# Kernel tuning notes

Hardware: AMD Instinct MI355X
Metric: run time of the kernel (lower is better)

Reference implementation:

```python
import jax, jax.numpy as jnp
import numpy as np

B, N, HID = 2, 512, 768
BIAF = 256
CLS = 14
CH = 32
SIZE_DIM = 25
N_POS = 30
HSZ = 2 * (BIAF + 1) + SIZE_DIM


def setup_inputs() -> dict:
    key = jax.random.key(0)
    ks = jax.random.split(key, 16)
    s = 0.02
    return {
        "x": jax.random.normal(ks[0], (B, N, HID), jnp.float32),
        "y": jax.random.normal(ks[1], (B, N, HID), jnp.float32),
        "z": jax.random.normal(ks[2], (B, N, N, CH), jnp.float32),
        "mlp1_w": jax.random.normal(ks[3], (BIAF, HID), jnp.float32) * s,
        "mlp1_b": jnp.zeros((BIAF,), jnp.float32),
        "mlp2_w": jax.random.normal(ks[4], (BIAF, HID), jnp.float32) * s,
        "mlp2_b": jnp.zeros((BIAF,), jnp.float32),
        "head_w": jax.random.normal(ks[5], (BIAF, HID), jnp.float32) * s,
        "head_b": jnp.zeros((BIAF,), jnp.float32),
        "tail_w": jax.random.normal(ks[6], (BIAF, HID), jnp.float32) * s,
        "tail_b": jnp.zeros((BIAF,), jnp.float32),
        "biaf_W": jax.random.normal(ks[7], (CLS, BIAF + 1, BIAF + 1), jnp.float32) * s,
        "W": jax.random.normal(ks[8], (CLS, HSZ), jnp.float32) * s,
        "size_emb": jax.random.normal(ks[9], (N_POS, SIZE_DIM), jnp.float32) * s,
    }


def reference(x, y, z, mlp1_w, mlp1_b, mlp2_w, mlp2_b, head_w, head_b,
              tail_w, tail_b, biaf_W, W, size_emb):
    # MLP branches (dropout=0 at eval; torch GELU is exact erf)
    h = jax.nn.gelu(x @ mlp1_w.T + mlp1_b, approximate=False)   # (b,m,BIAF)
    t = jax.nn.gelu(y @ mlp2_w.T + mlp2_b, approximate=False)   # (b,n,BIAF)
    ones = jnp.ones(h.shape[:-1] + (1,), h.dtype)
    h1 = jnp.concatenate([h, ones], -1)                          # (b,m,BIAF+1)
    t1 = jnp.concatenate([t, ones], -1)                          # (b,n,BIAF+1)
    # Biaffine with bias_x=bias_y=True -> (b,cls,m,n)
    o1 = jnp.einsum('bmi,kij,bnj->bkmn', h1, biaf_W, t1)

    # head/tail MLPs with LeakyReLU(0.01), then append 1-column
    head = jax.nn.leaky_relu(x @ head_w.T + head_b, 0.01)
    tail = jax.nn.leaky_relu(x @ tail_w.T + tail_b, 0.01)
    head = jnp.concatenate([head, ones], -1)                     # (b,m,BIAF+1)
    tail = jnp.concatenate([tail, ones], -1)                     # (b,n,BIAF+1)

    # einsum('bmnh,kh->bkmn', cat([head_m, tail_n, size_mn]), W) decomposed so
    # the (b,m,n,HSZ) pairwise tensor is never materialized (same math).
    d = head.shape[-1]
    Wh, Wt, Ws = W[:, :d], W[:, d:2 * d], W[:, 2 * d:]
    n = x.shape[1]
    ar = jnp.arange(n)
    ids = jnp.clip(ar[None, :] - ar[:, None], -N_POS // 2, N_POS // 2 - 1) + N_POS // 2
    se = size_emb[ids]                                           # (m,n,SIZE_DIM)
    o3 = (jnp.einsum('bmh,kh->bkm', head, Wh)[:, :, :, None]
          + jnp.einsum('bnh,kh->bkn', tail, Wt)[:, :, None, :]
          + jnp.einsum('mnh,kh->kmn', se, Ws)[None])
    return o1 + o3
```

## Files before the change

kernel.cpp:

```cpp
#include <hip/hip_runtime.h>
#include <hip/hip_bf16.h>
#include <math.h>
#include <stdint.h>

#define BDIM 2
#define NDIM 512
#define HID 768
#define BIAF 256
#define CLS 14
#define DD 257
#define NPOS 30
#define SDIM 25
#define HSZ 539
#define PK 288
#define PJ 384

typedef unsigned short ushort_t;
typedef __attribute__((ext_vector_type(8))) short short8;
typedef __attribute__((ext_vector_type(4))) float floatx4;
typedef __attribute__((ext_vector_type(4))) unsigned short ushort4_t;

#define MFMA16(a, b, c) __builtin_amdgcn_mfma_f32_16x16x32_bf16((a), (b), (c), 0, 0, 0)

__device__ inline float bf2f(ushort_t u) {
    union { unsigned int i; float f; } c; c.i = ((unsigned)u) << 16; return c.f;
}
__device__ inline ushort_t f2bf(float f) {
    __hip_bfloat16 h = __float2bfloat16(f);
    return *(ushort_t*)&h;
}

__device__ inline int xcd_swz(int bid, int nwg) {
    int q = nwg >> 3;
    return (bid & 7) * q + (bid >> 3);
}

__device__ inline void glds16(const ushort_t* g, const ushort_t* l) {
    __builtin_amdgcn_global_load_lds(
        (const __attribute__((address_space(1))) unsigned int*)(unsigned long long)(uintptr_t)g,
        (__attribute__((address_space(3))) unsigned int*)(unsigned int)(uintptr_t)l,
        16, 0, 0);
}


__global__ __launch_bounds__(256) void prep_all(
    const float* __restrict__ biafW, ushort_t* __restrict__ packW,
    const float* __restrict__ x, const float* __restrict__ y,
    const float* __restrict__ m1w, const float* __restrict__ m2w,
    const float* __restrict__ hw,  const float* __restrict__ tw,
    ushort_t* __restrict__ xhi, ushort_t* __restrict__ xlo,
    ushort_t* __restrict__ yhi, ushort_t* __restrict__ ylo,
    ushort_t* __restrict__ whi, ushort_t* __restrict__ wlo,
    ushort_t* __restrict__ h1hi, ushort_t* __restrict__ h1lo,
    ushort_t* __restrict__ t1hi, ushort_t* __restrict__ t1lo)
{
    const int bid = blockIdx.x;
    if (bid < 1512) {
        __shared__ float tile[32][33];
        const int ix = bid % 9;
        const int jy = (bid / 9) % 12;
        const int k  = bid / 108;
        const int i0 = ix * 32, j0 = jy * 32;
        const int r8 = threadIdx.x >> 5;
        const int c  = threadIdx.x & 31;
        #pragma unroll
        for (int rr = 0; rr < 4; ++rr) {
            int r = rr * 8 + r8;
            int gi = i0 + r, gj = j0 + c;
            tile[r][c] = (gi < DD && gj < DD) ? biafW[((size_t)k * DD + gi) * DD + gj] : 0.f;
        }
        __syncthreads();
        #pragma unroll
        for (int rr = 0; rr < 4; ++rr) {
            int jr = rr * 8 + r8;
            packW[((size_t)k * PJ + (j0 + jr)) * PK + i0 + c] = f2bf(tile[c][jr]);
        }
        return;
    }
    int tg = (bid - 1512) * 256 + threadIdx.x;
    if (tg < 196608) {
        int mat = tg / 49152;
        int e0  = (tg % 49152) * 4;
        const float* src = (mat == 0) ? m1w : (mat == 1) ? m2w : (mat == 2) ? hw : tw;
        float4 v = *(const float4*)(src + e0);
        size_t o = (size_t)mat * 196608 + e0;
        ushort4_t h, lo;
        h[0] = f2bf(v.x); lo[0] = f2bf(v.x - bf2f(h[0]));
        h[1] = f2bf(v.y); lo[1] = f2bf(v.y - bf2f(h[1]));
        h[2] = f2bf(v.z); lo[2] = f2bf(v.z - bf2f(h[2]));
        h[3] = f2bf(v.w); lo[3] = f2bf(v.w - bf2f(h[3]));
        *(ushort4_t*)(whi + o) = h;
        *(ushort4_t*)(wlo + o) = lo;
    } else if (tg < 589824) {
        int t = tg - 196608;
        int which = t / 196608;
        int e0 = (t % 196608) * 4;
        const float* src = which ? y : x;
        float4 v = *(const float4*)(src + e0);
        ushort4_t h, lo;
        h[0] = f2bf(v.x); lo[0] = f2bf(v.x - bf2f(h[0]));
        h[1] = f2bf(v.y); lo[1] = f2bf(v.y - bf2f(h[1]));
        h[2] = f2bf(v.z); lo[2] = f2bf(v.z - bf2f(h[2]));
        h[3] = f2bf(v.w); lo[3] = f2bf(v.w - bf2f(h[3]));
        *(ushort4_t*)((which ? yhi : xhi) + e0) = h;
        *(ushort4_t*)((which ? ylo : xlo) + e0) = lo;
    } else {
        int idx = tg - 589824;
        int plane = idx >> 15;
        int tok = (idx >> 5) & 1023;
        int c   = 256 + (idx & 31);
        ushort_t* dst = (plane == 0) ? h1hi : (plane == 1) ? h1lo : (plane == 2) ? t1hi : t1lo;
        ushort_t val = (c == 256 && (plane == 0 || plane == 2)) ? (ushort_t)0x3F80 : (ushort_t)0;
        dst[(size_t)tok * PK + c] = val;
    }
}

__global__ __launch_bounds__(256) void proj_mfma(
    const ushort_t* __restrict__ xhi, const ushort_t* __restrict__ xlo,
    const ushort_t* __restrict__ yhi, const ushort_t* __restrict__ ylo,
    const ushort_t* __restrict__ whi, const ushort_t* __restrict__ wlo,
    const float* __restrict__ m1b, const float* __restrict__ m2b,
    const float* __restrict__ hb,  const float* __restrict__ tb,
    ushort_t* __restrict__ h1hi, ushort_t* __restrict__ h1lo,
    ushort_t* __restrict__ t1hi, ushort_t* __restrict__ t1lo,
    float* __restrict__ headf, float* __restrict__ tailf)
{
    __shared__ __align__(16) ushort_t Sh[2 * 6144];
    const int flat = xcd_swz(blockIdx.x, 512);
    const int ft = flat & 7;
    const int mt = (flat >> 3) & 15;
    const int proj = flat >> 7;
    const int wave = threadIdx.x >> 6, L = threadIdx.x & 63;
    const int quad = L >> 4, l16 = L & 15;
    const int sr = L >> 3, u = (L & 7) ^ sr;
    const int srow = 2 * sr + (u >> 2);
    const int scol = (u & 3) * 8;
    const int rbase = (l16 >> 1) * 64 + (((((l16 & 1) << 2) | quad) ^ (l16 >> 1)) * 8);
    const int tok0 = mt * 64 + wave * 16;
    const int f0 = ft * 32;

    const ushort_t* ahi_p = (proj == 1) ? yhi : xhi;
    const ushort_t* alo_p = (proj == 1) ? ylo : xlo;
    const float* bias = (proj == 0) ? m1b : (proj == 1) ? m2b : (proj == 2) ? hb : tb;

    const ushort_t* gAh = ahi_p + (size_t)(mt * 64) * HID;
    const ushort_t* gAl = alo_p + (size_t)(mt * 64) * HID;
    const size_t wbase = (size_t)proj * BIAF * HID;
    const ushort_t* gWh = whi + wbase + (size_t)f0 * HID;
    const ushort_t* gWl = wlo + wbase + (size_t)f0 * HID;

    auto stage = [&](int bo, int k0) {
        for (int s = wave; s < 12; s += 4) {
            const ushort_t* g;
            if (s < 4)       g = gAh + (size_t)(s * 16 + srow) * HID + k0 + scol;
            else if (s < 8)  g = gAl + (size_t)((s - 4) * 16 + srow) * HID + k0 + scol;
            else if (s < 10) g = gWh + (size_t)((s - 8) * 16 + srow) * HID + k0 + scol;
            else             g = gWl + (size_t)((s - 10) * 16 + srow) * HID + k0 + scol;
            glds16(g, Sh + bo * 6144 + s * 512);
        }
    };

    floatx4 acc0 = {0.f, 0.f, 0.f, 0.f}, acc1 = {0.f, 0.f, 0.f, 0.f};
    stage(0, 0);
    __syncthreads();
    int cur = 0;
    for (int t = 0; t < 24; ++t) {
        if (t < 23) stage(cur ^ 1, (t + 1) * 32);
        const ushort_t* B = Sh + cur * 6144;
        short8 ah  = *(const short8*)(B + wave * 512 + rbase);
        short8 al  = *(const short8*)(B + 2048 + wave * 512 + rbase);
        short8 bh0 = *(const short8*)(B + 4096 + rbase);
        short8 bh1 = *(const short8*)(B + 4608 + rbase);
        short8 bl0 = *(const short8*)(B + 5120 + rbase);
        short8 bl1 = *(const short8*)(B + 5632 + rbase);
        acc0 = MFMA16(ah, bh0, acc0);
        acc1 = MFMA16(ah, bh1, acc1);
        acc0 = MFMA16(al, bh0, acc0);
        acc1 = MFMA16(al, bh1, acc1);
        acc0 = MFMA16(ah, bl0, acc0);
        acc1 = MFMA16(ah, bl1, acc1);
        __syncthreads();
        cur ^= 1;
    }

    #pragma unroll
    for (int nf = 0; nf < 2; ++nf) {
        floatx4 a = nf ? acc1 : acc0;
        int feat = f0 + nf * 16 + l16;
        float bv = bias[feat];
        #pragma unroll
        for (int r = 0; r < 4; ++r) {
            int tok = tok0 + quad * 4 + r;
            float v = a[r] + bv;
            if (proj <= 1) {
                float g = 0.5f * v * (1.0f + erff(v * 0.70710678118654752f));
                ushort_t h = f2bf(g);
                ushort_t lo = f2bf(g - bf2f(h));
                if (proj == 0) { h1hi[(size_t)tok * PK + feat] = h; h1lo[(size_t)tok * PK + feat] = lo; }
                else           { t1hi[(size_t)tok * PK + feat] = h; t1lo[(size_t)tok * PK + feat] = lo; }
            } else {
                float lv = (v >= 0.f) ? v : 0.01f * v;
                if (proj == 2) headf[(size_t)tok * 256 + feat] = lv;
                else           tailf[(size_t)tok * 256 + feat] = lv;
            }
        }
    }
}

__global__ __launch_bounds__(256) void mb_hk(
    const ushort_t* __restrict__ h1hi, const ushort_t* __restrict__ h1lo,
    const ushort_t* __restrict__ packW,
    ushort_t* __restrict__ Ab,
    const float* __restrict__ headf, const float* __restrict__ tailf,
    const float* __restrict__ W, const float* __restrict__ semb,
    float* __restrict__ hk, float* __restrict__ tk, float* __restrict__ skp)
{
    const int bid = blockIdx.x;
    if (bid >= 672) {
        const int hb = bid - 672;
        if (hb >= 128) {
            int idx = (hb - 128) * 256 + threadIdx.x;
            if (idx < CLS * NPOS) {
                int k = idx / NPOS, d = idx % NPOS;
                float acc = 0.f;
                for (int h = 0; h < SDIM; ++h)
                    acc += semb[d*SDIM + h] * W[k*HSZ + 2*DD + h];
                skp[idx] = acc;
            }
            return;
        }
        int p = hb * 256 + threadIdx.x;
        int which = p >> 14;
        int idx = p & 16383;
        int tok = idx >> 4;
        int k = idx & 15;
        if (k >= CLS) return;
        const float* row = (which ? tailf : headf) + (size_t)tok * 256;
        const float* wr = W + (size_t)k * HSZ + (which ? DD : 0);
        float acc = 0.f;
        for (int f4 = 0; f4 < 64; ++f4) {
            float4 rv = *(const float4*)(row + f4 * 4);
            acc += rv.x * wr[f4*4] + rv.y * wr[f4*4+1] + rv.z * wr[f4*4+2] + rv.w * wr[f4*4+3];
        }
        acc += wr[256];
        float* dst = which ? tk : hk;
        dst[(size_t)(tok >> 9) * CLS * NDIM + (size_t)k * NDIM + (tok & 511)] = acc;
        return;
    }

    __shared__ ushort_t Ah[2 * 2048];
    __shared__ ushort_t Al[2 * 2048];
    __shared__ ushort_t Bt[2 * 3072];
    const int flat = xcd_swz(bid, 672);
    const int jt = flat % 3, mt = (flat / 3) % 8, bk = flat / 24;
    const int b = bk / CLS, k = bk % CLS;
    const int tid = threadIdx.x;
    const int wave = tid >> 6, L = tid & 63;
    const int quad = L >> 4, l16 = L & 15;
    const int sr = L >> 3, u = (L & 7) ^ sr;
    const int srow = 2 * sr + (u >> 2);
    const int scol = (u & 3) * 8;
    const int rbase = (l16 >> 1) * 64 + ((((((l16 & 1) << 2) | quad)) ^ (l16 >> 1)) * 8);
    const int m0 = mt * 64, j0 = jt * 96;
    const int wm = (wave >> 1) * 32, wj = (wave & 1) * 48;

    const ushort_t* gAh = h1hi + (size_t)(b * NDIM + m0) * PK;
    const ushort_t* gAl = h1lo + (size_t)(b * NDIM + m0) * PK;
    const ushort_t* gB  = packW + ((size_t)k * PJ + j0) * PK;

    auto stage = [&](int bo, int k0) {
        for (int s = wave; s < 14; s += 4) {
            const ushort_t* g; const ushort_t* l;
            if (s < 4)      { l = Ah + bo * 2048 + s * 512;       g = gAh + (size_t)(s * 16 + srow) * PK + k0 + scol; }
            else if (s < 8) { l = Al + bo * 2048 + (s - 4) * 512; g = gAl + (size_t)((s - 4) * 16 + srow) * PK + k0 + scol; }
            else            { l = Bt + bo * 3072 + (s - 8) * 512; g = gB  + (size_t)((s - 8) * 16 + srow) * PK + k0 + scol; }
            glds16(g, l);
        }
    };

    floatx4 acc[2][3];
    #pragma unroll
    for (int mi = 0; mi < 2; ++mi)
        #pragma unroll
        for (int ni = 0; ni < 3; ++ni)
            #pragma unroll
            for (int r = 0; r < 4; ++r) acc[mi][ni][r] = 0.f;

    stage(0, 0);
    __syncthreads();
    int cur = 0;
    for (int t = 0; t < 9; ++t) {
        if (t < 8) stage(cur ^ 1, (t + 1) * 32);
        short8 ah[2], al[2], bb[3];
        #pragma unroll
        for (int mi = 0; mi < 2; ++mi) {
            ah[mi] = *(const short8*)(Ah + cur * 2048 + (wm + mi * 16) * 32 + rbase);
            al[mi] = *(const short8*)(Al + cur * 2048 + (wm + mi * 16) * 32 + rbase);
        }
        #pragma unroll
        for (int ni = 0; ni < 3; ++ni)
            bb[ni] = *(const short8*)(Bt + cur * 3072 + (wj + ni * 16) * 32 + rbase);
        #pragma unroll
        for (int mi = 0; mi < 2; ++mi)
            #pragma unroll
            for (int ni = 0; ni < 3; ++ni) {
                acc[mi][ni] = MFMA16(ah[mi], bb[ni], acc[mi][ni]);
                acc[mi][ni] = MFMA16(al[mi], bb[ni], acc[mi][ni]);
            }
        __syncthreads();
        cur ^= 1;
    }

    ushort_t* Aout = Ab + (size_t)bk * NDIM * PK;
    #pragma unroll
    for (int mi = 0; mi < 2; ++mi) {
        #pragma unroll
        for (int r = 0; r < 4; ++r) {
            int row = m0 + wm + mi * 16 + quad * 4 + r;
            #pragma unroll
            for (int ni = 0; ni < 3; ++ni) {
                int col = j0 + wj + ni * 16 + l16;
                Aout[(size_t)row * PK + col] = f2bf(acc[mi][ni][r]);
            }
        }
    }
}

__global__ __launch_bounds__(256) void mo_tile(
    const ushort_t* __restrict__ Ab,
    const ushort_t* __restrict__ t1hi, const ushort_t* __restrict__ t1lo,
    const float* __restrict__ hk, const float* __restrict__ tk,
    const float* __restrict__ sk,
    float* __restrict__ out)
{
    __shared__ ushort_t At[2 * 2048];
    __shared__ ushort_t Bh[2 * 4096];
    __shared__ ushort_t Bl[2 * 4096];
    __shared__ float skr[NPOS];
    const int flat = xcd_swz(blockIdx.x, 896);
    const int nt = flat & 3, mt = (flat >> 2) & 7, bk = flat >> 5;
    const int b = bk / CLS, k = bk % CLS;
    const int tid = threadIdx.x;
    if (tid < NPOS) skr[tid] = sk[k * NPOS + tid];
    const int wave = tid >> 6, L = tid & 63;
    const int quad = L >> 4, l16 = L & 15;
    const int sr = L >> 3, u = (L & 7) ^ sr;
    const int srow = 2 * sr + (u >> 2);
    const int scol = (u & 3) * 8;
    const int rbase = (l16 >> 1) * 64 + ((((((l16 & 1) << 2) | quad)) ^ (l16 >> 1)) * 8);
    const int m0 = mt * 64, n0 = nt * 128;
    const int wm = (wave >> 1) * 32, wn = (wave & 1) * 64;

    const ushort_t* gA  = Ab + ((size_t)bk * NDIM + m0) * PK;
    const ushort_t* gBh = t1hi + (size_t)(b * NDIM + n0) * PK;
    const ushort_t* gBl = t1lo + (size_t)(b * NDIM + n0) * PK;

    auto stage = [&](int bo, int k0) {
        for (int s = wave; s < 20; s += 4) {
            const ushort_t* g; const ushort_t* l;
            if (s < 4)       { l = At + bo * 2048 + s * 512;         g = gA  + (size_t)(s * 16 + srow) * PK + k0 + scol; }
            else if (s < 12) { l = Bh + bo * 4096 + (s - 4) * 512;   g = gBh + (size_t)((s - 4) * 16 + srow) * PK + k0 + scol; }
            else             { l = Bl + bo * 4096 + (s - 12) * 512;  g = gBl + (size_t)((s - 12) * 16 + srow) * PK + k0 + scol; }
            glds16(g, l);
        }
    };

    floatx4 acc[2][4];
    #pragma unroll
    for (int mi = 0; mi < 2; ++mi)
        #pragma unroll
        for (int ni = 0; ni < 4; ++ni)
            #pragma unroll
            for (int r = 0; r < 4; ++r) acc[mi][ni][r] = 0.f;

    stage(0, 0);
    __syncthreads();
    int cur = 0;
    for (int t = 0; t < 9; ++t) {
        if (t < 8) stage(cur ^ 1, (t + 1) * 32);
        short8 a[2], bh[4], bl[4];
        #pragma unroll
        for (int mi = 0; mi < 2; ++mi)
            a[mi] = *(const short8*)(At + cur * 2048 + (wm + mi * 16) * 32 + rbase);
        #pragma unroll
        for (int ni = 0; ni < 4; ++ni) {
            bh[ni] = *(const short8*)(Bh + cur * 4096 + (wn + ni * 16) * 32 + rbase);
            bl[ni] = *(const short8*)(Bl + cur * 4096 + (wn + ni * 16) * 32 + rbase);
        }
        #pragma unroll
        for (int mi = 0; mi < 2; ++mi)
            #pragma unroll
            for (int ni = 0; ni < 4; ++ni) {
                acc[mi][ni] = MFMA16(a[mi], bh[ni], acc[mi][ni]);
                acc[mi][ni] = MFMA16(a[mi], bl[ni], acc[mi][ni]);
            }
        __syncthreads();
        cur ^= 1;
    }

    const size_t obase = (size_t)bk * NDIM;
    #pragma unroll
    for (int mi = 0; mi < 2; ++mi) {
        #pragma unroll
        for (int r = 0; r < 4; ++r) {
            int row = m0 + wm + mi * 16 + quad * 4 + r;
            float hv = hk[obase + row];
            #pragma unroll
            for (int ni = 0; ni < 4; ++ni) {
                int col = n0 + wn + ni * 16 + l16;
                int d = col - row; d = d < -15 ? -15 : (d > 14 ? 14 : d); d += 15;
                out[(obase + row) * NDIM + col] = acc[mi][ni][r] + hv + tk[obase + col] + skr[d];
            }
        }
    }
}

extern "C" void kernel_launch(void* const* d_in, const int* in_sizes, int n_in,
                              void* d_out, int out_size, void* d_ws, size_t ws_size,
                              hipStream_t stream) {
    const float* x    = (const float*)d_in[0];
    const float* y    = (const float*)d_in[1];
    const float* m1w  = (const float*)d_in[3];
    const float* m1b  = (const float*)d_in[4];
    const float* m2w  = (const float*)d_in[5];
    const float* m2b  = (const float*)d_in[6];
    const float* hw   = (const float*)d_in[7];
    const float* hb   = (const float*)d_in[8];
    const float* tw   = (const float*)d_in[9];
    const float* tb   = (const float*)d_in[10];
    const float* biafW= (const float*)d_in[11];
    const float* W    = (const float*)d_in[12];
    const float* semb = (const float*)d_in[13];

    char* p = (char*)d_ws;
    float* hk   = (float*)p;                    p += 57344;
    float* tk   = (float*)p;                    p += 57344;
    float* skp  = (float*)p;                    p += 2048;
    float* headf= (float*)p;                    p += 1048576;
    float* tailf= (float*)p;                    p += 1048576;
    ushort_t* h1hi = (ushort_t*)p;              p += 589824;
    ushort_t* h1lo = (ushort_t*)p;              p += 589824;
    ushort_t* t1hi = (ushort_t*)p;              p += 589824;
    ushort_t* t1lo = (ushort_t*)p;              p += 589824;
    ushort_t* packW= (ushort_t*)p;              p += 3096576;
    ushort_t* whi  = (ushort_t*)p;              p += 1572864;
    ushort_t* wlo  = (ushort_t*)p;              p += 1572864;
    ushort_t* Abuf = (ushort_t*)p;              p += 8257536;
    ushort_t* xhi  = (ushort_t*)p;              p += 1572864;
    ushort_t* xlo  = (ushort_t*)p;              p += 1572864;
    ushort_t* yhi  = (ushort_t*)p;              p += 1572864;
    ushort_t* ylo  = (ushort_t*)p;              p += 1572864;

    prep_all<<<4328, 256, 0, stream>>>(biafW, packW, x, y, m1w, m2w, hw, tw,
                                       xhi, xlo, yhi, ylo, whi, wlo,
                                       h1hi, h1lo, t1hi, t1lo);
    proj_mfma<<<512, 256, 0, stream>>>(xhi, xlo, yhi, ylo, whi, wlo,
                                       m1b, m2b, hb, tb,
                                       h1hi, h1lo, t1hi, t1lo, headf, tailf);
    mb_hk<<<802, 256, 0, stream>>>(h1hi, h1lo, packW, Abuf,
                                   headf, tailf, W, semb, hk, tk, skp);
    mo_tile<<<896, 256, 0, stream>>>(Abuf, t1hi, t1lo, hk, tk, skp,
                                     (float*)d_out);
}
```

Baseline: 180.1 us.

## Fuse bf16 hi/lo split into projection GEMM and merge prep kernels

```diff
diff --git a/kernel.cpp b/kernel.cpp
--- a/kernel.cpp
+++ b/kernel.cpp
@@ -43,129 +43,124 @@
 }
 
 
-__global__ __launch_bounds__(256) void prep_all(
-    const float* __restrict__ biafW, ushort_t* __restrict__ packW,
+__global__ __launch_bounds__(256) void prep_proj(
     const float* __restrict__ x, const float* __restrict__ y,
     const float* __restrict__ m1w, const float* __restrict__ m2w,
     const float* __restrict__ hw,  const float* __restrict__ tw,
-    ushort_t* __restrict__ xhi, ushort_t* __restrict__ xlo,
-    ushort_t* __restrict__ yhi, ushort_t* __restrict__ ylo,
-    ushort_t* __restrict__ whi, ushort_t* __restrict__ wlo,
+    const float* __restrict__ m1b, const float* __restrict__ m2b,
+    const float* __restrict__ hb,  const float* __restrict__ tb,
+    const float* __restrict__ biafW, ushort_t* __restrict__ packW,
     ushort_t* __restrict__ h1hi, ushort_t* __restrict__ h1lo,
-    ushort_t* __restrict__ t1hi, ushort_t* __restrict__ t1lo)
+    ushort_t* __restrict__ t1hi, ushort_t* __restrict__ t1lo,
+    float* __restrict__ headf, float* __restrict__ tailf)
 {
+    __shared__ __align__(16) ushort_t Sh[2 * 6144];
     const int bid = blockIdx.x;
-    if (bid < 1512) {
-        __shared__ float tile[32][33];
-        const int ix = bid % 9;
-        const int jy = (bid / 9) % 12;
-        const int k  = bid / 108;
-        const int i0 = ix * 32, j0 = jy * 32;
-        const int r8 = threadIdx.x >> 5;
-        const int c  = threadIdx.x & 31;
-        #pragma unroll
-        for (int rr = 0; rr < 4; ++rr) {
-            int r = rr * 8 + r8;
-            int gi = i0 + r, gj = j0 + c;
-            tile[r][c] = (gi < DD && gj < DD) ? biafW[((size_t)k * DD + gi) * DD + gj] : 0.f;
-        }
-        __syncthreads();
-        #pragma unroll
-        for (int rr = 0; rr < 4; ++rr) {
-            int jr = rr * 8 + r8;
-            packW[((size_t)k * PJ + (j0 + jr)) * PK + i0 + c] = f2bf(tile[c][jr]);
-        }
-        return;
-    }
-    int tg = (bid - 1512) * 256 + threadIdx.x;
-    if (tg < 196608) {
-        int mat = tg / 49152;
-        int e0  = (tg % 49152) * 4;
-        const float* src = (mat == 0) ? m1w : (mat == 1) ? m2w : (mat == 2) ? hw : tw;
-        float4 v = *(const float4*)(src + e0);
-        size_t o = (size_t)mat * 196608 + e0;
-        ushort4_t h, lo;
-        h[0] = f2bf(v.x); lo[0] = f2bf(v.x - bf2f(h[0]));
-        h[1] = f2bf(v.y); lo[1] = f2bf(v.y - bf2f(h[1]));
-        h[2] = f2bf(v.z); lo[2] = f2bf(v.z - bf2f(h[2]));
-        h[3] = f2bf(v.w); lo[3] = f2bf(v.w - bf2f(h[3]));
-        *(ushort4_t*)(whi + o) = h;
-        *(ushort4_t*)(wlo + o) = lo;
-    } else if (tg < 589824) {
-        int t = tg - 196608;
-        int which = t / 196608;
-        int e0 = (t % 196608) * 4;
-        const float* src = which ? y : x;
-        float4 v = *(const float4*)(src + e0);
-        ushort4_t h, lo;
-        h[0] = f2bf(v.x); lo[0] = f2bf(v.x - bf2f(h[0]));
-        h[1] = f2bf(v.y); lo[1] = f2bf(v.y - bf2f(h[1]));
-        h[2] = f2bf(v.z); lo[2] = f2bf(v.z - bf2f(h[2]));
-        h[3] = f2bf(v.w); lo[3] = f2bf(v.w - bf2f(h[3]));
-        *(ushort4_t*)((which ? yhi : xhi) + e0) = h;
-        *(ushort4_t*)((which ? ylo : xlo) + e0) = lo;
-    } else {
-        int idx = tg - 589824;
+    const int tid = threadIdx.x;
+
+    if (bid >= 2024) {
+        int idx = (bid - 2024) * 256 + tid;
         int plane = idx >> 15;
         int tok = (idx >> 5) & 1023;
         int c   = 256 + (idx & 31);
         ushort_t* dst = (plane == 0) ? h1hi : (plane == 1) ? h1lo : (plane == 2) ? t1hi : t1lo;
         ushort_t val = (c == 256 && (plane == 0 || plane == 2)) ? (ushort_t)0x3F80 : (ushort_t)0;
         dst[(size_t)tok * PK + c] = val;
-    }
-}
-
-__global__ __launch_bounds__(256) void proj_mfma(
-    const ushort_t* __restrict__ xhi, const ushort_t* __restrict__ xlo,
-    const ushort_t* __restrict__ yhi, const ushort_t* __restrict__ ylo,
-    const ushort_t* __restrict__ whi, const ushort_t* __restrict__ wlo,
-    const float* __restrict__ m1b, const float* __restrict__ m2b,
-    const float* __restrict__ hb,  const float* __restrict__ tb,
-    ushort_t* __restrict__ h1hi, ushort_t* __restrict__ h1lo,
-    ushort_t* __restrict__ t1hi, ushort_t* __restrict__ t1lo,
-    float* __restrict__ headf, float* __restrict__ tailf)
-{
-    __shared__ __align__(16) ushort_t Sh[2 * 6144];
-    const int flat = xcd_swz(blockIdx.x, 512);
+        return;
+    }
+    if (bid >= 512) {
+        float (*tile)[33] = reinterpret_cast<float(*)[33]>(Sh);
+        const int rb = bid - 512;
+        const int ix = rb % 9;
+        const int jy = (rb / 9) % 12;
+        const int k  = rb / 108;
+        const int i0 = ix * 32, j0 = jy * 32;
+        const int r8 = tid >> 5;
+        const int c  = tid & 31;
+        #pragma unroll
+        for (int rr = 0; rr < 4; ++rr) {
+            int r = rr * 8 + r8;
+            int gi = i0 + r, gj = j0 + c;
+            tile[r][c] = (gi < DD && gj < DD) ? biafW[((size_t)k * DD + gi) * DD + gj] : 0.f;
+        }
+        __syncthreads();
+        #pragma unroll
+        for (int rr = 0; rr < 4; ++rr) {
+            int jr = rr * 8 + r8;
+            packW[((size_t)k * PJ + (j0 + jr)) * PK + i0 + c] = f2bf(tile[c][jr]);
+        }
+        return;
+    }
+
+    const int flat = xcd_swz(bid, 512);
     const int ft = flat & 7;
     const int mt = (flat >> 3) & 15;
     const int proj = flat >> 7;
-    const int wave = threadIdx.x >> 6, L = threadIdx.x & 63;
+    const int wave = tid >> 6, L = tid & 63;
     const int quad = L >> 4, l16 = L & 15;
-    const int sr = L >> 3, u = (L & 7) ^ sr;
-    const int srow = 2 * sr + (u >> 2);
-    const int scol = (u & 3) * 8;
     const int rbase = (l16 >> 1) * 64 + (((((l16 & 1) << 2) | quad) ^ (l16 >> 1)) * 8);
     const int tok0 = mt * 64 + wave * 16;
     const int f0 = ft * 32;
 
-    const ushort_t* ahi_p = (proj == 1) ? yhi : xhi;
-    const ushort_t* alo_p = (proj == 1) ? ylo : xlo;
+    const int ar = L >> 2, acq = L & 3;
+    const int aoffe = ((ar >> 1) * 64) + (((((ar & 1) << 2) | acq) ^ ((ar >> 1) & 7)) * 8);
+    const int fr = tid >> 3, wc4 = (tid & 7) * 4;
+    const int wseg = fr >> 4, wr = fr & 15;
+    const int woffe = ((wr >> 1) * 64) + (((((wr & 1) << 2) | (wc4 >> 3)) ^ ((wr >> 1) & 7)) * 8) + (wc4 & 7);
+
+    const float* asrc = (proj == 1) ? y : x;
+    const float* wsrc = (proj == 0) ? m1w : (proj == 1) ? m2w : (proj == 2) ? hw : tw;
     const float* bias = (proj == 0) ? m1b : (proj == 1) ? m2b : (proj == 2) ? hb : tb;
-
-    const ushort_t* gAh = ahi_p + (size_t)(mt * 64) * HID;
-    const ushort_t* gAl = alo_p + (size_t)(mt * 64) * HID;
-    const size_t wbase = (size_t)proj * BIAF * HID;
-    const ushort_t* gWh = whi + wbase + (size_t)f0 * HID;
-    const ushort_t* gWl = wlo + wbase + (size_t)f0 * HID;
-
-    auto stage = [&](int bo, int k0) {
-        for (int s = wave; s < 12; s += 4) {
-            const ushort_t* g;
-            if (s < 4)       g = gAh + (size_t)(s * 16 + srow) * HID + k0 + scol;
-            else if (s < 8)  g = gAl + (size_t)((s - 4) * 16 + srow) * HID + k0 + scol;
-            else if (s < 10) g = gWh + (size_t)((s - 8) * 16 + srow) * HID + k0 + scol;
-            else             g = gWl + (size_t)((s - 10) * 16 + srow) * HID + k0 + scol;
-            glds16(g, Sh + bo * 6144 + s * 512);
-        }
+    const float* aptr = asrc + (size_t)(mt * 64 + wave * 16 + ar) * HID + acq * 8;
+    const float* wptr = wsrc + (size_t)(f0 + fr) * HID + wc4;
+
+    auto cvt_write = [&](int bo, float4 a0, float4 a1, float4 wv) {
+        ushort_t* B = Sh + bo * 6144;
+        float av[8] = {a0.x, a0.y, a0.z, a0.w, a1.x, a1.y, a1.z, a1.w};
+        short8 hh, ll;
+        #pragma unroll
+        for (int j = 0; j < 8; ++j) {
+            ushort_t h = f2bf(av[j]);
+            hh[j] = (short)h;
+            ll[j] = (short)f2bf(av[j] - bf2f(h));
+        }
+        *(short8*)(B + wave * 512 + aoffe) = hh;
+        *(short8*)(B + 2048 + wave * 512 + aoffe) = ll;
+        float wvv[4] = {wv.x, wv.y, wv.z, wv.w};
+        ushort4_t wh, wl;
+        #pragma unroll
+        for (int j = 0; j < 4; ++j) {
+            ushort_t h = f2bf(wvv[j]);
+            wh[j] = h;
+            wl[j] = f2bf(wvv[j] - bf2f(h));
+        }
+        *(ushort4_t*)(B + 4096 + wseg * 512 + woffe) = wh;
+        *(ushort4_t*)(B + 5120 + wseg * 512 + woffe) = wl;
     };
 
     floatx4 acc0 = {0.f, 0.f, 0.f, 0.f}, acc1 = {0.f, 0.f, 0.f, 0.f};
-    stage(0, 0);
+
+    float4 pa0 = *(const float4*)(aptr);
+    float4 pa1 = *(const float4*)(aptr + 4);
+    float4 pw  = *(const float4*)(wptr);
+    cvt_write(0, pa0, pa1, pw);
+    pa0 = *(const float4*)(aptr + 32);
+    pa1 = *(const float4*)(aptr + 36);
+    pw  = *(const float4*)(wptr + 32);
     __syncthreads();
+
     int cur = 0;
+    #pragma unroll 2
     for (int t = 0; t < 24; ++t) {
-        if (t < 23) stage(cur ^ 1, (t + 1) * 32);
+        if (t < 23) {
+            cvt_write(cur ^ 1, pa0, pa1, pw);
+            if (t < 22) {
+                int k2 = (t + 2) * 32;
+                pa0 = *(const float4*)(aptr + k2);
+                pa1 = *(const float4*)(aptr + k2 + 4);
+                pw  = *(const float4*)(wptr + k2);
+            }
+        }
         const ushort_t* B = Sh + cur * 6144;
         short8 ah  = *(const short8*)(B + wave * 512 + rbase);
         short8 al  = *(const short8*)(B + 2048 + wave * 512 + rbase);
@@ -443,20 +438,12 @@
     ushort_t* t1hi = (ushort_t*)p;              p += 589824;
     ushort_t* t1lo = (ushort_t*)p;              p += 589824;
     ushort_t* packW= (ushort_t*)p;              p += 3096576;
-    ushort_t* whi  = (ushort_t*)p;              p += 1572864;
-    ushort_t* wlo  = (ushort_t*)p;              p += 1572864;
     ushort_t* Abuf = (ushort_t*)p;              p += 8257536;
-    ushort_t* xhi  = (ushort_t*)p;              p += 1572864;
-    ushort_t* xlo  = (ushort_t*)p;              p += 1572864;
-    ushort_t* yhi  = (ushort_t*)p;              p += 1572864;
-    ushort_t* ylo  = (ushort_t*)p;              p += 1572864;
-
-    prep_all<<<4328, 256, 0, stream>>>(biafW, packW, x, y, m1w, m2w, hw, tw,
-                                       xhi, xlo, yhi, ylo, whi, wlo,
-                                       h1hi, h1lo, t1hi, t1lo);
-    proj_mfma<<<512, 256, 0, stream>>>(xhi, xlo, yhi, ylo, whi, wlo,
-                                       m1b, m2b, hb, tb,
-                                       h1hi, h1lo, t1hi, t1lo, headf, tailf);
+
+    prep_proj<<<2536, 256, 0, stream>>>(x, y, m1w, m2w, hw, tw,
+                                        m1b, m2b, hb, tb,
+                                        biafW, packW,
+                                        h1hi, h1lo, t1hi, t1lo, headf, tailf);
     mb_hk<<<802, 256, 0, stream>>>(h1hi, h1lo, packW, Abuf,
                                    headf, tailf, W, semb, hk, tk, skp);
     mo_tile<<<896, 256, 0, stream>>>(Abuf, t1hi, t1lo, hk, tk, skp,
```

Measured after the change: 177.3 us. About the same (-1.5%).
